# Kernel tuning notes

Hardware: AMD Instinct MI355X
Metric: run time of the kernel (lower is better)

## Reference

```python
import jax, jax.numpy as jnp
import numpy as np

B, S, H, NH = 2, 2048, 2048, 16
HD = H // NH  # 128


def setup_inputs() -> dict:
    key = jax.random.key(0)
    ks = jax.random.split(key, 6)
    x = jax.random.normal(ks[0], (B, S, H), dtype=jnp.float32)
    # causal additive mask: 0 on/below diagonal, -1e9 above
    causal = jnp.triu(jnp.full((S, S), -1e9, dtype=jnp.float32), k=1)
    attention_mask = causal[None, None, :, :]  # [1,1,S,S]
    # ALiBi: per-head slope * key position, broadcast over queries
    slopes = 2.0 ** (-8.0 * (jnp.arange(NH, dtype=jnp.float32) + 1) / NH)
    alibi = (-slopes[:, None] * jnp.arange(S, dtype=jnp.float32)[None, :])
    alibi = alibi[None, :, None, :]  # [1,NH,1,S]
    scale = 0.02
    Wq = jax.random.normal(ks[1], (H, H), dtype=jnp.float32) * scale
    Wk = jax.random.normal(ks[2], (H, H), dtype=jnp.float32) * scale
    Wv = jax.random.normal(ks[3], (H, H), dtype=jnp.float32) * scale
    Wo = jax.random.normal(ks[4], (H, H), dtype=jnp.float32) * scale
    return {"x": x, "attention_mask": attention_mask, "alibi": alibi,
            "Wq": Wq, "Wk": Wk, "Wv": Wv, "Wo": Wo}


def reference(x, attention_mask, alibi, Wq, Wk, Wv, Wo):
    b, s, _ = x.shape
    # nn.Linear(y) = y @ W.T
    q = (x @ Wq.T).reshape(b, s, NH, HD).transpose(0, 2, 1, 3)  # [b,h,s,d]
    k = (x @ Wk.T).reshape(b, s, NH, HD).transpose(0, 2, 1, 3)
    v = (x @ Wv.T).reshape(b, s, NH, HD).transpose(0, 2, 1, 3)
    scores = jnp.einsum('bhqd,bhkd->bhqk', q, k) / jnp.sqrt(jnp.float32(HD))
    scores = scores + alibi + attention_mask
    attn = jax.nn.softmax(scores, axis=-1)
    out = jnp.einsum('bhqk,bhkd->bhqd', attn, v)
    out = out.transpose(0, 2, 1, 3).reshape(b, s, H)
    return out @ Wo.T
```

## Files before the change

kernel.cpp:

```cpp
#include <hip/hip_runtime.h>

typedef unsigned short u16;
typedef float f32x4 __attribute__((ext_vector_type(4)));
typedef short s16x8 __attribute__((ext_vector_type(8)));
typedef short s16x4 __attribute__((ext_vector_type(4)));
typedef unsigned short u16x4 __attribute__((ext_vector_type(4)));

#define S_LEN 2048
#define HDIM 2048
#define NHEADS 16
#define HEAD_DIM 128

__device__ __forceinline__ u16 f2bf(float f) {
    unsigned u = __builtin_bit_cast(unsigned, f);
    u += 0x7FFFu + ((u >> 16) & 1u);
    return (u16)(u >> 16);
}

__device__ __forceinline__ void gload_lds16(const u16* g, u16* l) {
    __builtin_amdgcn_global_load_lds(
        (const __attribute__((address_space(1))) unsigned int*)(const void*)g,
        (__attribute__((address_space(3))) unsigned int*)(void*)l, 16, 0, 0);
}

#define PBAR __builtin_amdgcn_s_barrier()
#define SGB0 __builtin_amdgcn_sched_barrier(0)

__device__ __forceinline__ void tr_read16(const u16* bptr, s16x4* o) {
    auto p = (const __attribute__((address_space(3))) u16*)(const void*)bptr;
    asm volatile(
        "ds_read_b64_tr_b16 %0, %16\n\t"
        "ds_read_b64_tr_b16 %1, %16 offset:1024\n\t"
        "ds_read_b64_tr_b16 %2, %16 offset:128\n\t"
        "ds_read_b64_tr_b16 %3, %16 offset:1152\n\t"
        "ds_read_b64_tr_b16 %4, %16 offset:256\n\t"
        "ds_read_b64_tr_b16 %5, %16 offset:1280\n\t"
        "ds_read_b64_tr_b16 %6, %16 offset:384\n\t"
        "ds_read_b64_tr_b16 %7, %16 offset:1408\n\t"
        "ds_read_b64_tr_b16 %8, %16 offset:512\n\t"
        "ds_read_b64_tr_b16 %9, %16 offset:1536\n\t"
        "ds_read_b64_tr_b16 %10, %16 offset:640\n\t"
        "ds_read_b64_tr_b16 %11, %16 offset:1664\n\t"
        "ds_read_b64_tr_b16 %12, %16 offset:768\n\t"
        "ds_read_b64_tr_b16 %13, %16 offset:1792\n\t"
        "ds_read_b64_tr_b16 %14, %16 offset:896\n\t"
        "ds_read_b64_tr_b16 %15, %16 offset:1920\n\t"
        "s_waitcnt lgkmcnt(0)"
        : "=&v"(o[0]), "=&v"(o[1]), "=&v"(o[2]), "=&v"(o[3]),
          "=&v"(o[4]), "=&v"(o[5]), "=&v"(o[6]), "=&v"(o[7]),
          "=&v"(o[8]), "=&v"(o[9]), "=&v"(o[10]), "=&v"(o[11]),
          "=&v"(o[12]), "=&v"(o[13]), "=&v"(o[14]), "=&v"(o[15])
        : "v"(p));
    __builtin_amdgcn_sched_barrier(0);
}

__global__ void cvt_bf16(const float* __restrict__ in, u16* __restrict__ out, int n4, float scale) {
    int i = blockIdx.x * blockDim.x + threadIdx.x;
    int stride = gridDim.x * blockDim.x;
    for (; i < n4; i += stride) {
        float4 f = ((const float4*)in)[i];
        u16x4 r;
        r.x = f2bf(f.x * scale); r.y = f2bf(f.y * scale);
        r.z = f2bf(f.z * scale); r.w = f2bf(f.w * scale);
        *(u16x4*)(out + (size_t)i * 4) = r;
    }
}

__global__ void cvt_w4(const float* __restrict__ w0, const float* __restrict__ w1,
                       const float* __restrict__ w2, const float* __restrict__ w3,
                       u16* __restrict__ out, float scale0) {
    const int n4each = (HDIM * HDIM) / 4;
    int b = blockIdx.x;
    int which = b >> 11;
    const float* src = which == 0 ? w0 : which == 1 ? w1 : which == 2 ? w2 : w3;
    float sc = which == 0 ? scale0 : 1.0f;
    u16* dst = out + (size_t)which * (HDIM * HDIM);
    int i = (b & 2047) * 256 + threadIdx.x;
    const int stride = 2048 * 256;
    for (; i < n4each; i += stride) {
        float4 f = ((const float4*)src)[i];
        u16x4 r;
        r.x = f2bf(f.x * sc); r.y = f2bf(f.y * sc);
        r.z = f2bf(f.z * sc); r.w = f2bf(f.w * sc);
        *(u16x4*)(dst + (size_t)i * 4) = r;
    }
}

__global__ __launch_bounds__(512, 2) void gemm_qkv(const u16* __restrict__ A, const u16* __restrict__ Bw,
                                                   u16* __restrict__ C0, u16* __restrict__ C1,
                                                   u16* __restrict__ C2, int M, int N, int K) {
    __shared__ u16 lds[2][28672];

    const int bid = blockIdx.x;
    const int xcd = bid & 7;
    const int q = bid >> 3;
    const int bm = xcd * 2 + (q & 1);
    const int bn = q >> 1;

    const int t = threadIdx.x, lane = t & 63, w = t >> 6;
    const int wm = w >> 1, wn = w & 1;
    const int rqg = lane >> 4, rl = lane & 15;

    const size_t rowA0 = (size_t)bm * 256;
    const int colB0 = bn * 192;

    const u16* srcA[4]; int dA[4];
#pragma unroll
    for (int i = 0; i < 4; ++i) {
        int c = t + i * 512;
        int row = c >> 3, ch = c & 7;
        srcA[i] = A + (rowA0 + row) * (size_t)K + ((ch ^ (row & 7)) << 3);
        dA[i] = c * 8;
    }
    const u16* srcB[3]; int dB[3];
#pragma unroll
    for (int i = 0; i < 3; ++i) {
        int c = t + i * 512;
        int row = c >> 3, ch = c & 7;
        srcB[i] = Bw + (size_t)(colB0 + row) * (size_t)K + ((ch ^ (row & 7)) << 3);
        dB[i] = 16384 + c * 8;
    }

    auto stage = [&](int tile, int side) {
        const size_t go = (size_t)tile * 64;
        u16* base = &lds[side][0];
#pragma unroll
        for (int i = 0; i < 4; ++i) gload_lds16(srcA[i] + go, base + dA[i]);
#pragma unroll
        for (int i = 0; i < 3; ++i) gload_lds16(srcB[i] + go, base + dB[i]);
    };

    const int chv[2] = { ((0 + rqg) ^ (rl & 7)) << 3, ((4 + rqg) ^ (rl & 7)) << 3 };
    const int arow = wm * 64, brow = wn * 96;

    f32x4 acc[4][6] = {};

    const int NT = K >> 6;

    stage(0, 0); stage(1, 1);
    asm volatile("s_waitcnt vmcnt(7)" ::: "memory");
    PBAR;

    for (int tt = 0; tt < NT; ++tt) {
        const int side = tt & 1;
        const u16* sA = &lds[side][0];
        const u16* sB = sA + 16384;

        s16x8 af[4][2], bf[6][2];
#pragma unroll
        for (int m = 0; m < 4; ++m)
#pragma unroll
            for (int k = 0; k < 2; ++k)
                af[m][k] = *(const s16x8*)&sA[(arow + m * 16 + rl) * 64 + chv[k]];
#pragma unroll
        for (int n = 0; n < 6; ++n)
#pragma unroll
            for (int k = 0; k < 2; ++k)
                bf[n][k] = *(const s16x8*)&sB[(brow + n * 16 + rl) * 64 + chv[k]];

        asm volatile("s_waitcnt lgkmcnt(0)" ::: "memory");
        SGB0;
        PBAR;
        SGB0;
        if (tt + 2 < NT) stage(tt + 2, side);

        __builtin_amdgcn_s_setprio(1);
#pragma unroll
        for (int m = 0; m < 4; ++m)
#pragma unroll
            for (int n = 0; n < 6; ++n)
#pragma unroll
                for (int k = 0; k < 2; ++k)
                    acc[m][n] = __builtin_amdgcn_mfma_f32_16x16x32_bf16(af[m][k], bf[n][k], acc[m][n], 0, 0, 0);
        __builtin_amdgcn_s_setprio(0);

        if (tt + 2 < NT)      { asm volatile("s_waitcnt vmcnt(7)" ::: "memory"); }
        else if (tt + 1 < NT) { asm volatile("s_waitcnt vmcnt(0)" ::: "memory"); }
        PBAR;
    }

#pragma unroll
    for (int m = 0; m < 4; ++m) {
#pragma unroll
        for (int n = 0; n < 6; ++n) {
            int colg = colB0 + wn * 96 + n * 16;
            int mat = colg >> 11;
            u16* Csel = mat == 0 ? C0 : mat == 1 ? C1 : C2;
            int colm = (colg & 2047) + rl;
#pragma unroll
            for (int j = 0; j < 4; ++j) {
                size_t row = rowA0 + wm * 64 + m * 16 + rqg * 4 + j;
                Csel[row * 2048 + colm] = f2bf(acc[m][n][j]);
            }
        }
    }
}

__global__ __launch_bounds__(512, 2) void gemm_wo(const u16* __restrict__ A, const u16* __restrict__ Bw,
                                                  float* __restrict__ C, int M, int N, int K) {
    __shared__ u16 lds[3 * 24576];

    const int bid = blockIdx.x;
    const int xcd = bid & 7;
    const int q = bid >> 3;
    const int rr = q & 31, sc0 = q >> 5;
    const int bm = xcd * 4 + (rr & 3);
    const int bn = sc0 * 8 + (rr >> 2);

    const int t = threadIdx.x, lane = t & 63, w = t >> 6;
    const int wm = w >> 2, wn = w & 3;
    const int rqg = lane >> 4, rl = lane & 15;

    const size_t rowA0 = (size_t)bm * 128;
    const int colB0 = bn << 8;

    const u16* srcA[2]; int dA[2];
#pragma unroll
    for (int i = 0; i < 2; ++i) {
        int c = t + i * 512;
        int row = c >> 3, ch = c & 7;
        srcA[i] = A + (rowA0 + row) * (size_t)K + ((ch ^ (row & 7)) << 3);
        dA[i] = c * 8;
    }
    const u16* srcB[4]; int dB[4];
#pragma unroll
    for (int i = 0; i < 4; ++i) {
        int c = t + i * 512;
        int row = c >> 3, ch = c & 7;
        srcB[i] = Bw + (size_t)(colB0 + row) * (size_t)K + ((ch ^ (row & 7)) << 3);
        dB[i] = c * 8;
    }

    auto stage = [&](int tile, int s) {
        const size_t go = (size_t)tile * 64;
        u16* base = &lds[s * 24576];
#pragma unroll
        for (int i = 0; i < 2; ++i) gload_lds16(srcA[i] + go, base + dA[i]);
#pragma unroll
        for (int i = 0; i < 4; ++i) gload_lds16(srcB[i] + go, base + 8192 + dB[i]);
    };

    const int chv[2] = { ((0 + rqg) ^ (rl & 7)) << 3, ((4 + rqg) ^ (rl & 7)) << 3 };
    const int arow = wm * 64, brow = wn * 64;

    f32x4 acc[4][4] = {};

    const int NT = K >> 6;

    stage(0, 0); stage(1, 1);
    asm volatile("s_waitcnt vmcnt(6)" ::: "memory");
    PBAR;

    int s = 0;
    for (int tt = 0; tt < NT; ++tt) {
        const u16* sA = &lds[s * 24576];
        const u16* sB = sA + 8192;

        s16x8 af[4][2], bf[4][2];
#pragma unroll
        for (int m = 0; m < 4; ++m)
#pragma unroll
            for (int k = 0; k < 2; ++k)
                af[m][k] = *(const s16x8*)&sA[(arow + m * 16 + rl) * 64 + chv[k]];
#pragma unroll
        for (int n = 0; n < 4; ++n)
#pragma unroll
            for (int k = 0; k < 2; ++k)
                bf[n][k] = *(const s16x8*)&sB[(brow + n * 16 + rl) * 64 + chv[k]];

        int s2 = s + 2; if (s2 >= 3) s2 -= 3;
        if (tt + 2 < NT) stage(tt + 2, s2);
        SGB0;
        asm volatile("s_waitcnt lgkmcnt(0)" ::: "memory");
        SGB0;

        __builtin_amdgcn_s_setprio(1);
#pragma unroll
        for (int m = 0; m < 4; ++m)
#pragma unroll
            for (int n = 0; n < 4; ++n)
#pragma unroll
                for (int k = 0; k < 2; ++k)
                    acc[m][n] = __builtin_amdgcn_mfma_f32_16x16x32_bf16(af[m][k], bf[n][k], acc[m][n], 0, 0, 0);
        __builtin_amdgcn_s_setprio(0);

        if (tt + 2 < NT)      { asm volatile("s_waitcnt vmcnt(6)" ::: "memory"); }
        else if (tt + 1 < NT) { asm volatile("s_waitcnt vmcnt(0)" ::: "memory"); }
        PBAR;
        ++s; if (s == 3) s = 0;
    }

#pragma unroll
    for (int m = 0; m < 4; ++m) {
#pragma unroll
        for (int n = 0; n < 4; ++n) {
#pragma unroll
            for (int j = 0; j < 4; ++j) {
                size_t row = rowA0 + wm * 64 + m * 16 + rqg * 4 + j;
                size_t col = colB0 + wn * 64 + n * 16 + rl;
                C[row * 2048 + col] = acc[m][n][j];
            }
        }
    }
}

__global__ __launch_bounds__(512) void attn_kernel(const u16* __restrict__ Q, const u16* __restrict__ Kb,
                                                   const u16* __restrict__ Vb,
                                                   const float* __restrict__ alibi,
                                                   u16* __restrict__ O) {
    __shared__ u16 ldsKV[3 * 16384];
    __shared__ u16 lP[8][16 * 80];

    const int bid = blockIdx.x;
    const int bh = bid & 31;
    const int p = bid >> 5;
    const int h = bh & 15, b = bh >> 4;
    const int t = threadIdx.x, lane = t & 63, w = t >> 6;
    const int rqg = lane >> 4, rl = lane & 15;

    const size_t bS = (size_t)b * S_LEN;
    const size_t hOff = (size_t)h * HEAD_DIM;

    const u16* ksrc[2]; const u16* vsrc[2]; int cdst[2];
#pragma unroll
    for (int i = 0; i < 2; ++i) {
        int c = t + i * 512;
        int krow = c >> 4, kch = c & 15;
        ksrc[i] = Kb + (bS + krow) * HDIM + hOff + ((kch ^ (krow & 7)) << 3);
        int vkey = ((c >> 6) << 2) + ((c >> 1) & 3);
        int vd = (((c >> 3) & 7) << 4) + ((c & 1) << 3);
        vsrc[i] = Vb + (bS + vkey) * HDIM + hOff + vd;
        cdst[i] = c * 8;
    }

    auto stageKV = [&](int tile, int s) {
        const size_t goff = (size_t)tile * 64 * HDIM;
        u16* base = &ldsKV[s * 16384];
#pragma unroll
        for (int i = 0; i < 2; ++i) {
            gload_lds16(ksrc[i] + goff, base + cdst[i]);
            gload_lds16(vsrc[i] + goff, base + 8192 + cdst[i]);
        }
    };

    const float mslope2 = alibi[(size_t)h * S_LEN + 1] * 1.4426950408889634f;

    s16x8 ones;
#pragma unroll
    for (int i = 0; i < 8; ++i) ones[i] = (short)0x3F80;

    for (int sidx = 0; sidx < 2; ++sidx) {
        const int qt = sidx ? (15 - p) : p;
        const int q0w = qt * 128 + w * 16;

        const size_t baseQ = (bS + q0w + rl) * HDIM + hOff;
        s16x8 qf[4];
#pragma unroll
        for (int kk = 0; kk < 4; ++kk)
            qf[kk] = *(const s16x8*)(Q + baseQ + kk * 32 + rqg * 8);

        float m[4];
        f32x4 o[8]; f32x4 osum = {0.f, 0.f, 0.f, 0.f};
#pragma unroll
        for (int j = 0; j < 4; ++j) m[j] = -1e30f;
#pragma unroll
        for (int n = 0; n < 8; ++n) o[n] = (f32x4){0.f, 0.f, 0.f, 0.f};

        const int nkt = 2 * qt + 2;
        const int my_last = 2 * qt + (w >> 2);
        u16* lPw = lP[w];

        stageKV(0, 0); stageKV(1, 1);
        asm volatile("s_waitcnt vmcnt(4)" ::: "memory");
        PBAR;

        int s = 0;
        for (int kt = 0; kt < nkt; ++kt) {
            int s2 = s + 2; if (s2 >= 3) s2 -= 3;
            if (kt + 2 < nkt) stageKV(kt + 2, s2);

            if (kt <= my_last) {
                const int k0 = kt * 64;
                const u16* kbase = &ldsKV[s * 16384];

                f32x4 sfr[4] = {};
#pragma unroll
                for (int kk = 0; kk < 4; ++kk) {
#pragma unroll
                    for (int nt = 0; nt < 4; ++nt) {
                        int row = nt * 16 + rl;
                        int off = row * 256 + ((kk * 64 + rqg * 16) ^ ((row & 7) << 4));
                        s16x8 kf = *(const s16x8*)((const char*)kbase + off);
                        sfr[nt] = __builtin_amdgcn_mfma_f32_16x16x32_bf16(qf[kk], kf, sfr[nt], 0, 0, 0);
                    }
                }

                const bool diag = (kt == my_last);
                float scv[4][4];
                float thr0 = m[0] + 8.f, thr1 = m[1] + 8.f, thr2 = m[2] + 8.f, thr3 = m[3] + 8.f;
                int small = 1;
#pragma unroll
                for (int nt = 0; nt < 4; ++nt) {
                    int key = k0 + nt * 16 + rl;
                    float al = mslope2 * (float)key;
#pragma unroll
                    for (int j = 0; j < 4; ++j) {
                        float v = sfr[nt][j] + al;
                        if (diag) {
                            int qrow = q0w + rqg * 4 + j;
                            v = (key <= qrow) ? v : -1e30f;
                        }
                        scv[nt][j] = v;
                        float thr = (j == 0) ? thr0 : (j == 1) ? thr1 : (j == 2) ? thr2 : thr3;
                        small &= (v <= thr) ? 1 : 0;
                    }
                }
                if (!__all(small)) {
                    float rmax[4];
#pragma unroll
                    for (int j = 0; j < 4; ++j)
                        rmax[j] = fmaxf(fmaxf(scv[0][j], scv[1][j]), fmaxf(scv[2][j], scv[3][j]));
#pragma unroll
                    for (int off = 1; off < 16; off <<= 1) {
#pragma unroll
                        for (int j = 0; j < 4; ++j) rmax[j] = fmaxf(rmax[j], __shfl_xor(rmax[j], off));
                    }
#pragma unroll
                    for (int j = 0; j < 4; ++j) {
                        float mn = fmaxf(m[j], rmax[j]);
                        float fac = exp2f(m[j] - mn);
                        m[j] = mn;
                        osum[j] *= fac;
#pragma unroll
                        for (int n = 0; n < 8; ++n) o[n][j] *= fac;
                    }
                }

#pragma unroll
                for (int nt = 0; nt < 4; ++nt) {
#pragma unroll
                    for (int j = 0; j < 4; ++j) {
                        float pv = exp2f(scv[nt][j] - m[j]);
                        lPw[(rqg * 4 + j) * 80 + nt * 16 + rl] = f2bf(pv);
                    }
                }

                const u16* lVbase = &ldsKV[s * 16384] + 8192 + rqg * 1024 + rl * 4;
#pragma unroll
                for (int kk = 0; kk < 2; ++kk) {
                    s16x8 pf = *(const s16x8*)&lPw[rl * 80 + kk * 32 + rqg * 8];
                    osum = __builtin_amdgcn_mfma_f32_16x16x32_bf16(pf, ones, osum, 0, 0, 0);
                    s16x4 tr[16];
                    tr_read16(lVbase + kk * 4096, tr);
#pragma unroll
                    for (int n = 0; n < 8; ++n) {
                        s16x8 vf = __builtin_shufflevector(tr[2 * n], tr[2 * n + 1], 0, 1, 2, 3, 4, 5, 6, 7);
                        o[n] = __builtin_amdgcn_mfma_f32_16x16x32_bf16(pf, vf, o[n], 0, 0, 0);
                    }
                }
            }

            if (kt + 2 < nkt)      { asm volatile("s_waitcnt vmcnt(4)" ::: "memory"); }
            else if (kt + 1 < nkt) { asm volatile("s_waitcnt vmcnt(0)" ::: "memory"); }
            PBAR;
            ++s; if (s == 3) s = 0;
        }

        float inv[4];
#pragma unroll
        for (int j = 0; j < 4; ++j) inv[j] = 1.0f / osum[j];
#pragma unroll
        for (int n = 0; n < 8; ++n) {
#pragma unroll
            for (int j = 0; j < 4; ++j) {
                size_t row = bS + q0w + rqg * 4 + j;
                O[row * HDIM + hOff + n * 16 + rl] = f2bf(o[n][j] * inv[j]);
            }
        }
    }
}

extern "C" void kernel_launch(void* const* d_in, const int* in_sizes, int n_in,
                              void* d_out, int out_size, void* d_ws, size_t ws_size,
                              hipStream_t stream) {
    (void)in_sizes; (void)n_in; (void)out_size; (void)ws_size;
    const float* x     = (const float*)d_in[0];
    const float* alibi = (const float*)d_in[2];
    const float* Wq    = (const float*)d_in[3];
    const float* Wk    = (const float*)d_in[4];
    const float* Wv    = (const float*)d_in[5];
    const float* Wo    = (const float*)d_in[6];
    float* out = (float*)d_out;

    char* ws = (char*)d_ws;
    u16* xb  = (u16*)(ws + 0);
    u16* wqb = (u16*)(ws + 16777216);
    u16* Qb  = (u16*)(ws + 50331648);
    u16* Kv  = Qb + 8388608;
    u16* Vv  = Kv + 8388608;
    u16* Ob  = Vv + 8388608;
    u16* wob = wqb + 3 * 4194304;

    const int M = 2 * S_LEN;
    const int K = HDIM;

    const float qscale = 0.08838834764831845f * 1.4426950408889634f;
    cvt_bf16<<<4096, 256, 0, stream>>>(x, xb, (2 * S_LEN * HDIM) / 4, 1.0f);
    cvt_w4<<<8192, 256, 0, stream>>>(Wq, Wk, Wv, Wo, wqb, qscale);

    gemm_qkv<<<(M / 256) * (3 * HDIM / 192), 512, 0, stream>>>(xb, wqb, Qb, Kv, Vv, M, 3 * HDIM, K);

    attn_kernel<<<2 * NHEADS * 8, 512, 0, stream>>>(Qb, Kv, Vv, alibi, Ob);

    gemm_wo<<<(M / 128) * (HDIM / 256), 512, 0, stream>>>(Ob, wob, out, M, HDIM, K);
}
```

Before: 243.4 us.

## Retile QKV GEMM to 128x256 with triple-buffered LDS and one barrier per step

Changes the QKV projection GEMM from 256x192 tiles with double-buffered LDS to 128x256 tiles with a three-slot LDS ring. The prefetch for tile t+2 is now issued right after fragment reads, with no extra barrier or LDS wait before it, so each k-step has one barrier instead of two. The block-to-tile mapping follows the XCD-aware scheme used by gemm_wo, and the epilogue picks the output matrix once per block. Trade-offs: a smaller per-wave accumulator tile lowers arithmetic intensity, and more LDS per block may limit occupancy.

```diff
diff --git a/kernel.cpp b/kernel.cpp
--- a/kernel.cpp
+++ b/kernel.cpp
@@ -89,108 +89,108 @@
 __global__ __launch_bounds__(512, 2) void gemm_qkv(const u16* __restrict__ A, const u16* __restrict__ Bw,
                                                    u16* __restrict__ C0, u16* __restrict__ C1,
                                                    u16* __restrict__ C2, int M, int N, int K) {
-    __shared__ u16 lds[2][28672];
+    __shared__ u16 lds[3 * 24576];
 
     const int bid = blockIdx.x;
     const int xcd = bid & 7;
     const int q = bid >> 3;
-    const int bm = xcd * 2 + (q & 1);
-    const int bn = q >> 1;
+    const int rr = q & 31, sc0 = q >> 5;
+    const int bm = xcd * 4 + (rr & 3);
+    const int bn = sc0 * 8 + (rr >> 2);
 
     const int t = threadIdx.x, lane = t & 63, w = t >> 6;
-    const int wm = w >> 1, wn = w & 1;
+    const int wm = w >> 2, wn = w & 3;
     const int rqg = lane >> 4, rl = lane & 15;
 
-    const size_t rowA0 = (size_t)bm * 256;
-    const int colB0 = bn * 192;
-
-    const u16* srcA[4]; int dA[4];
-#pragma unroll
-    for (int i = 0; i < 4; ++i) {
+    const size_t rowA0 = (size_t)bm * 128;
+    const int colB0 = bn << 8;
+
+    const u16* srcA[2]; int dA[2];
+#pragma unroll
+    for (int i = 0; i < 2; ++i) {
         int c = t + i * 512;
         int row = c >> 3, ch = c & 7;
         srcA[i] = A + (rowA0 + row) * (size_t)K + ((ch ^ (row & 7)) << 3);
         dA[i] = c * 8;
     }
-    const u16* srcB[3]; int dB[3];
-#pragma unroll
-    for (int i = 0; i < 3; ++i) {
+    const u16* srcB[4]; int dB[4];
+#pragma unroll
+    for (int i = 0; i < 4; ++i) {
         int c = t + i * 512;
         int row = c >> 3, ch = c & 7;
         srcB[i] = Bw + (size_t)(colB0 + row) * (size_t)K + ((ch ^ (row & 7)) << 3);
-        dB[i] = 16384 + c * 8;
-    }
-
-    auto stage = [&](int tile, int side) {
+        dB[i] = c * 8;
+    }
+
+    auto stage = [&](int tile, int s) {
         const size_t go = (size_t)tile * 64;
-        u16* base = &lds[side][0];
-#pragma unroll
-        for (int i = 0; i < 4; ++i) gload_lds16(srcA[i] + go, base + dA[i]);
-#pragma unroll
-        for (int i = 0; i < 3; ++i) gload_lds16(srcB[i] + go, base + dB[i]);
+        u16* base = &lds[s * 24576];
+#pragma unroll
+        for (int i = 0; i < 2; ++i) gload_lds16(srcA[i] + go, base + dA[i]);
+#pragma unroll
+        for (int i = 0; i < 4; ++i) gload_lds16(srcB[i] + go, base + 8192 + dB[i]);
     };
 
     const int chv[2] = { ((0 + rqg) ^ (rl & 7)) << 3, ((4 + rqg) ^ (rl & 7)) << 3 };
-    const int arow = wm * 64, brow = wn * 96;
-
-    f32x4 acc[4][6] = {};
+    const int arow = wm * 64, brow = wn * 64;
+
+    f32x4 acc[4][4] = {};
 
     const int NT = K >> 6;
 
     stage(0, 0); stage(1, 1);
-    asm volatile("s_waitcnt vmcnt(7)" ::: "memory");
+    asm volatile("s_waitcnt vmcnt(6)" ::: "memory");
     PBAR;
 
+    int s = 0;
     for (int tt = 0; tt < NT; ++tt) {
-        const int side = tt & 1;
-        const u16* sA = &lds[side][0];
-        const u16* sB = sA + 16384;
-
-        s16x8 af[4][2], bf[6][2];
+        const u16* sA = &lds[s * 24576];
+        const u16* sB = sA + 8192;
+
+        s16x8 af[4][2], bf[4][2];
 #pragma unroll
         for (int m = 0; m < 4; ++m)
 #pragma unroll
             for (int k = 0; k < 2; ++k)
                 af[m][k] = *(const s16x8*)&sA[(arow + m * 16 + rl) * 64 + chv[k]];
 #pragma unroll
-        for (int n = 0; n < 6; ++n)
+        for (int n = 0; n < 4; ++n)
 #pragma unroll
             for (int k = 0; k < 2; ++k)
                 bf[n][k] = *(const s16x8*)&sB[(brow + n * 16 + rl) * 64 + chv[k]];
 
-        asm volatile("s_waitcnt lgkmcnt(0)" ::: "memory");
+        int s2 = s + 2; if (s2 >= 3) s2 -= 3;
+        if (tt + 2 < NT) stage(tt + 2, s2);
         SGB0;
-        PBAR;
-        SGB0;
-        if (tt + 2 < NT) stage(tt + 2, side);
 
         __builtin_amdgcn_s_setprio(1);
 #pragma unroll
         for (int m = 0; m < 4; ++m)
 #pragma unroll
-            for (int n = 0; n < 6; ++n)
+            for (int n = 0; n < 4; ++n)
 #pragma unroll
                 for (int k = 0; k < 2; ++k)
                     acc[m][n] = __builtin_amdgcn_mfma_f32_16x16x32_bf16(af[m][k], bf[n][k], acc[m][n], 0, 0, 0);
         __builtin_amdgcn_s_setprio(0);
 
-        if (tt + 2 < NT)      { asm volatile("s_waitcnt vmcnt(7)" ::: "memory"); }
+        if (tt + 2 < NT)      { asm volatile("s_waitcnt vmcnt(6)" ::: "memory"); }
         else if (tt + 1 < NT) { asm volatile("s_waitcnt vmcnt(0)" ::: "memory"); }
         PBAR;
-    }
-
+        ++s; if (s == 3) s = 0;
+    }
+
+    const int mat = colB0 >> 11;
+    u16* Csel = mat == 0 ? C0 : mat == 1 ? C1 : C2;
+    const int colb = (colB0 & 2047) + wn * 64;
 #pragma unroll
     for (int m = 0; m < 4; ++m) {
 #pragma unroll
-        for (int n = 0; n < 6; ++n) {
-            int colg = colB0 + wn * 96 + n * 16;
-            int mat = colg >> 11;
-            u16* Csel = mat == 0 ? C0 : mat == 1 ? C1 : C2;
-            int colm = (colg & 2047) + rl;
+        for (int n = 0; n < 4; ++n) {
 #pragma unroll
             for (int j = 0; j < 4; ++j) {
                 size_t row = rowA0 + wm * 64 + m * 16 + rqg * 4 + j;
-                Csel[row * 2048 + colm] = f2bf(acc[m][n][j]);
+                size_t col = colb + n * 16 + rl;
+                Csel[row * 2048 + col] = f2bf(acc[m][n][j]);
             }
         }
     }
@@ -508,7 +508,7 @@
     cvt_bf16<<<4096, 256, 0, stream>>>(x, xb, (2 * S_LEN * HDIM) / 4, 1.0f);
     cvt_w4<<<8192, 256, 0, stream>>>(Wq, Wk, Wv, Wo, wqb, qscale);
 
-    gemm_qkv<<<(M / 256) * (3 * HDIM / 192), 512, 0, stream>>>(xb, wqb, Qb, Kv, Vv, M, 3 * HDIM, K);
+    gemm_qkv<<<(M / 128) * (3 * HDIM / 256), 512, 0, stream>>>(xb, wqb, Qb, Kv, Vv, M, 3 * HDIM, K);
 
     attn_kernel<<<2 * NHEADS * 8, 512, 0, stream>>>(Qb, Kv, Vv, alibi, Ob);
 
```

Result: slower. 255.2 us (median of 2 runs) (+4.9%).

## Restructure QKV GEMM to 256x384 tiles, 1024 threads, triple-buffered K=32 stages

Applied to the files above, without the earlier changes.

The QKV projection GEMM now uses 1024-thread blocks (16 waves in a 4x4 grid) computing 256x384 output tiles instead of 256x192. The K step shrinks from 64 to 32 and the LDS uses three rotating stages with a new XOR swizzle. The mid-loop barrier is removed, so the prefetch is issued right after the fragment reads. This aims to raise reuse of each A tile, cut barrier count per step, and deepen the load pipeline. In exchange it doubles the loop trip count, leaves far fewer blocks in the grid, and relies on per-wave vmcnt bookkeeping that differs by wave index.

```diff
diff --git a/kernel.cpp b/kernel.cpp
--- a/kernel.cpp
+++ b/kernel.cpp
@@ -86,10 +86,10 @@
     }
 }
 
-__global__ __launch_bounds__(512, 2) void gemm_qkv(const u16* __restrict__ A, const u16* __restrict__ Bw,
-                                                   u16* __restrict__ C0, u16* __restrict__ C1,
-                                                   u16* __restrict__ C2, int M, int N, int K) {
-    __shared__ u16 lds[2][28672];
+__global__ __launch_bounds__(1024, 4) void gemm_qkv(const u16* __restrict__ A, const u16* __restrict__ Bw,
+                                                    u16* __restrict__ C0, u16* __restrict__ C1,
+                                                    u16* __restrict__ C2, int M, int N, int K) {
+    __shared__ u16 lds[3 * 20480];
 
     const int bid = blockIdx.x;
     const int xcd = bid & 7;
@@ -98,85 +98,81 @@
     const int bn = q >> 1;
 
     const int t = threadIdx.x, lane = t & 63, w = t >> 6;
-    const int wm = w >> 1, wn = w & 1;
+    const int wm = w >> 2, wn = w & 3;
     const int rqg = lane >> 4, rl = lane & 15;
 
     const size_t rowA0 = (size_t)bm * 256;
-    const int colB0 = bn * 192;
-
-    const u16* srcA[4]; int dA[4];
-#pragma unroll
-    for (int i = 0; i < 4; ++i) {
-        int c = t + i * 512;
-        int row = c >> 3, ch = c & 7;
-        srcA[i] = A + (rowA0 + row) * (size_t)K + ((ch ^ (row & 7)) << 3);
-        dA[i] = c * 8;
-    }
-    const u16* srcB[3]; int dB[3];
-#pragma unroll
-    for (int i = 0; i < 3; ++i) {
-        int c = t + i * 512;
-        int row = c >> 3, ch = c & 7;
-        srcB[i] = Bw + (size_t)(colB0 + row) * (size_t)K + ((ch ^ (row & 7)) << 3);
-        dB[i] = 16384 + c * 8;
-    }
-
-    auto stage = [&](int tile, int side) {
-        const size_t go = (size_t)tile * 64;
-        u16* base = &lds[side][0];
-#pragma unroll
-        for (int i = 0; i < 4; ++i) gload_lds16(srcA[i] + go, base + dA[i]);
-#pragma unroll
-        for (int i = 0; i < 3; ++i) gload_lds16(srcB[i] + go, base + dB[i]);
+    const int colB0 = bn * 384;
+
+    const int rowA = t >> 2, chA = t & 3;
+    const u16* srcA = A + (rowA0 + rowA) * (size_t)K + ((chA ^ ((rowA >> 1) & 3)) << 3);
+    const int dA = t * 8;
+    const bool doB = (t < 768);
+    const u16* srcB0 = nullptr; const u16* srcB1 = nullptr; int dB0 = 0, dB1 = 0;
+    if (doB) {
+        int c0 = t, r0 = c0 >> 2, h0 = c0 & 3;
+        srcB0 = Bw + (size_t)(colB0 + r0) * (size_t)K + ((h0 ^ ((r0 >> 1) & 3)) << 3);
+        dB0 = 8192 + c0 * 8;
+        int c1 = t + 768, r1 = c1 >> 2, h1 = c1 & 3;
+        srcB1 = Bw + (size_t)(colB0 + r1) * (size_t)K + ((h1 ^ ((r1 >> 1) & 3)) << 3);
+        dB1 = 8192 + c1 * 8;
+    }
+
+    auto stage = [&](int tile, int s) {
+        const size_t go = (size_t)tile * 32;
+        u16* base = &lds[s * 20480];
+        gload_lds16(srcA + go, base + dA);
+        if (doB) {
+            gload_lds16(srcB0 + go, base + dB0);
+            gload_lds16(srcB1 + go, base + dB1);
+        }
     };
 
-    const int chv[2] = { ((0 + rqg) ^ (rl & 7)) << 3, ((4 + rqg) ^ (rl & 7)) << 3 };
+    auto wait_steady = [&]() {
+        if (w < 12) { asm volatile("s_waitcnt vmcnt(3)" ::: "memory"); }
+        else        { asm volatile("s_waitcnt vmcnt(1)" ::: "memory"); }
+    };
+
+    const int chf = (rqg ^ ((rl >> 1) & 3)) << 3;
     const int arow = wm * 64, brow = wn * 96;
 
     f32x4 acc[4][6] = {};
 
-    const int NT = K >> 6;
+    const int NT = K >> 5;
 
     stage(0, 0); stage(1, 1);
-    asm volatile("s_waitcnt vmcnt(7)" ::: "memory");
+    wait_steady();
     PBAR;
 
+    int s = 0;
     for (int tt = 0; tt < NT; ++tt) {
-        const int side = tt & 1;
-        const u16* sA = &lds[side][0];
-        const u16* sB = sA + 16384;
-
-        s16x8 af[4][2], bf[6][2];
+        const u16* sA = &lds[s * 20480];
+        const u16* sB = sA + 8192;
+
+        s16x8 af[4], bf[6];
 #pragma unroll
         for (int m = 0; m < 4; ++m)
-#pragma unroll
-            for (int k = 0; k < 2; ++k)
-                af[m][k] = *(const s16x8*)&sA[(arow + m * 16 + rl) * 64 + chv[k]];
+            af[m] = *(const s16x8*)&sA[(arow + m * 16 + rl) * 32 + chf];
 #pragma unroll
         for (int n = 0; n < 6; ++n)
-#pragma unroll
-            for (int k = 0; k < 2; ++k)
-                bf[n][k] = *(const s16x8*)&sB[(brow + n * 16 + rl) * 64 + chv[k]];
-
-        asm volatile("s_waitcnt lgkmcnt(0)" ::: "memory");
+            bf[n] = *(const s16x8*)&sB[(brow + n * 16 + rl) * 32 + chf];
+
+        int s2 = s + 2; if (s2 >= 3) s2 -= 3;
+        if (tt + 2 < NT) stage(tt + 2, s2);
         SGB0;
-        PBAR;
-        SGB0;
-        if (tt + 2 < NT) stage(tt + 2, side);
 
         __builtin_amdgcn_s_setprio(1);
 #pragma unroll
         for (int m = 0; m < 4; ++m)
 #pragma unroll
             for (int n = 0; n < 6; ++n)
-#pragma unroll
-                for (int k = 0; k < 2; ++k)
-                    acc[m][n] = __builtin_amdgcn_mfma_f32_16x16x32_bf16(af[m][k], bf[n][k], acc[m][n], 0, 0, 0);
+                acc[m][n] = __builtin_amdgcn_mfma_f32_16x16x32_bf16(af[m], bf[n], acc[m][n], 0, 0, 0);
         __builtin_amdgcn_s_setprio(0);
 
-        if (tt + 2 < NT)      { asm volatile("s_waitcnt vmcnt(7)" ::: "memory"); }
+        if (tt + 2 < NT)      { wait_steady(); }
         else if (tt + 1 < NT) { asm volatile("s_waitcnt vmcnt(0)" ::: "memory"); }
         PBAR;
+        ++s; if (s == 3) s = 0;
     }
 
 #pragma unroll
@@ -508,7 +504,7 @@
     cvt_bf16<<<4096, 256, 0, stream>>>(x, xb, (2 * S_LEN * HDIM) / 4, 1.0f);
     cvt_w4<<<8192, 256, 0, stream>>>(Wq, Wk, Wv, Wo, wqb, qscale);
 
-    gemm_qkv<<<(M / 256) * (3 * HDIM / 192), 512, 0, stream>>>(xb, wqb, Qb, Kv, Vv, M, 3 * HDIM, K);
+    gemm_qkv<<<(M / 256) * (3 * HDIM / 384), 1024, 0, stream>>>(xb, wqb, Qb, Kv, Vv, M, 3 * HDIM, K);
 
     attn_kernel<<<2 * NHEADS * 8, 512, 0, stream>>>(Qb, Kv, Vv, alibi, Ob);
 
```

After: 616.7 us. 153% more time.
